# Kernel optimization log

Measured on AMD Instinct MI355X. Metric: run time of the kernel, lower is better.

## Reference

```python
import jax, jax.numpy as jnp
import numpy as np

HIDDEN = 4544
N_HEADS = 71
HEAD_DIM = 64
SEQ = 2048
ROPE_BASE = 10000.0


def _rope_cos_sin(seq_len, dim, base=ROPE_BASE):
    inv_freq = 1.0 / (base ** (jnp.arange(0, dim, 2, dtype=jnp.float32) / dim))
    t = jnp.arange(seq_len, dtype=jnp.float32)
    freqs = jnp.einsum('i,j->ij', t, inv_freq)          # [s, dim/2]
    emb = jnp.concatenate([freqs, freqs], axis=-1)      # [s, dim]
    return jnp.cos(emb), jnp.sin(emb)


def _rotate_half(x):
    x1, x2 = jnp.split(x, 2, axis=-1)
    return jnp.concatenate([-x2, x1], axis=-1)


def _apply_rope(x, cos, sin):
    # x: [..., s, d]; cos/sin: [s, d] broadcast over leading dims
    return x * cos + _rotate_half(x) * sin


def setup_inputs() -> dict:
    key = jax.random.key(0)
    k1, k2, k3 = jax.random.split(key, 3)
    hidden_states = jax.random.normal(k1, (1, 1, SEQ, HIDDEN), dtype=jnp.float32) * 0.02
    qkv_weight = jax.random.normal(k2, ((N_HEADS + 2) * HEAD_DIM, HIDDEN), dtype=jnp.float32) * 0.02
    dense_weight = jax.random.normal(k3, (HIDDEN, HIDDEN), dtype=jnp.float32) * 0.02
    # causal additive mask, same construction as the torch module (triu of -1e5)
    mask = jnp.triu(jnp.full((SEQ, SEQ), -100000.0, dtype=jnp.float32), k=1)[None, None]
    return {
        'hidden_states': hidden_states,
        'qkv_weight': qkv_weight,
        'dense_weight': dense_weight,
        'attention_mask': mask,
    }


def reference(hidden_states, qkv_weight, dense_weight, attention_mask):
    b = hidden_states.shape[0]
    s = hidden_states.shape[2]
    x = hidden_states[:, 0]                                   # [b, s, H]

    # fused QKV projection (no bias): [b, s, (nH+2)*d]
    fused = jnp.einsum('bsh,oh->bso', x, qkv_weight)

    q = fused[..., : N_HEADS * HEAD_DIM]
    q = q.reshape(b, s, N_HEADS, HEAD_DIM).transpose(0, 2, 1, 3)   # [b, nH, s, d]
    k = fused[..., N_HEADS * HEAD_DIM : (N_HEADS + 1) * HEAD_DIM]  # [b, s, d] (single KV head, MQA)
    v = fused[..., (N_HEADS + 1) * HEAD_DIM :]                     # [b, s, d]

    cos, sin = _rope_cos_sin(s, HEAD_DIM)
    q = _apply_rope(q, cos, sin)
    k = _apply_rope(k, cos, sin)

    scale = 1.0 / np.sqrt(HEAD_DIM).astype(np.float32)
    scores = jnp.einsum('bhqd,bkd->bhqk', q, k) * scale            # [b, nH, s, s]
    scores = scores + attention_mask
    attn = jax.nn.softmax(scores, axis=-1)
    out = jnp.einsum('bhqk,bkd->bhqd', attn, v)                    # [b, nH, s, d]

    out = out.transpose(0, 2, 1, 3).reshape(b, s, N_HEADS * HEAD_DIM)  # concat heads
    out = jnp.einsum('bsh,oh->bso', out, dense_weight)             # dense projection
    return out[:, None]                                            # [b, 1, s, H]
```

## Files before the change

### kernel.cpp

```cpp
#include <hip/hip_runtime.h>

#define SEQ     2048
#define HIDDEN  4544
#define NHEAD   71
#define HD      64
#define QKV_OUT 4672

typedef __bf16    bf16;
typedef _Float16  f16;
typedef __bf16    bf16x8 __attribute__((ext_vector_type(8)));
typedef __bf16    bf16x4 __attribute__((ext_vector_type(4)));
typedef _Float16  f16x4  __attribute__((ext_vector_type(4)));
typedef _Float16  f16x8  __attribute__((ext_vector_type(8)));
typedef float     f32x4  __attribute__((ext_vector_type(4)));

__device__ inline void gl2lds16(const void* g, void* ldsbase) {
  __builtin_amdgcn_global_load_lds(
      (const __attribute__((address_space(1))) unsigned int*)g,
      (__attribute__((address_space(3))) unsigned int*)ldsbase,
      16, 0, 0);
}

__global__ void cvt_f32_bf16_k(const float* __restrict__ in, bf16* __restrict__ out, int n4) {
  int i = blockIdx.x * blockDim.x + threadIdx.x;
  if (i >= n4) return;
  float4 f = ((const float4*)in)[i];
  bf16x4 o;
  o[0] = (bf16)f.x; o[1] = (bf16)f.y; o[2] = (bf16)f.z; o[3] = (bf16)f.w;
  *(bf16x4*)(out + (size_t)i * 4) = o;
}

__global__ __launch_bounds__(256) void gemm_bt_k(const bf16* __restrict__ A,
                                                 const bf16* __restrict__ B,
                                                 float* __restrict__ C,
                                                 int K, int Nmat, int ldc) {
  __shared__ bf16 lA[2][128 * 32];
  __shared__ bf16 lB[2][128 * 32];
  const int t = threadIdx.x;
  const int lane = t & 63, w = t >> 6;

  const int gx = gridDim.x;
  const int nwg = gx * gridDim.y;
  const int orig = blockIdx.y * gx + blockIdx.x;
  const int swz = (orig & 7) * (nwg >> 3) + (orig >> 3);
  const int m0 = (swz % gx) * 128;
  const int n0 = (swz / gx) * 128;

  const int wm = (w >> 1) * 64, wn = (w & 1) * 64;
  const int qi = lane & 15, grp = lane >> 4;

  const int r0 = t >> 2;
  const int c0 = (t & 3) * 8;
  const bf16* gA0 = A + (size_t)(m0 + r0) * K + c0;
  const bf16* gA1 = A + (size_t)(m0 + 64 + r0) * K + c0;
  int bR0 = n0 + r0;      if (bR0 >= Nmat) bR0 = Nmat - 1;
  int bR1 = n0 + 64 + r0; if (bR1 >= Nmat) bR1 = Nmat - 1;
  const bf16* gB0 = B + (size_t)bR0 * K + c0;
  const bf16* gB1 = B + (size_t)bR1 * K + c0;
  bf16* lA00 = &lA[0][0] + w * 512;
  bf16* lA01 = &lA[0][2048] + w * 512;
  bf16* lA10 = &lA[1][0] + w * 512;
  bf16* lA11 = &lA[1][2048] + w * 512;
  bf16* lB00 = &lB[0][0] + w * 512;
  bf16* lB01 = &lB[0][2048] + w * 512;
  bf16* lB10 = &lB[1][0] + w * 512;
  bf16* lB11 = &lB[1][2048] + w * 512;

  f32x4 acc[4][4] = {};
  for (int k0 = 0; k0 < K; k0 += 64) {
    __syncthreads();
    gl2lds16(gA0 + k0,      lA00);
    gl2lds16(gA1 + k0,      lA01);
    gl2lds16(gA0 + k0 + 32, lA10);
    gl2lds16(gA1 + k0 + 32, lA11);
    gl2lds16(gB0 + k0,      lB00);
    gl2lds16(gB1 + k0,      lB01);
    gl2lds16(gB0 + k0 + 32, lB10);
    gl2lds16(gB1 + k0 + 32, lB11);
    __syncthreads();
#pragma unroll
    for (int half = 0; half < 2; ++half) {
      bf16x8 af[4], bfv[4];
#pragma unroll
      for (int i = 0; i < 4; ++i)
        af[i] = *(const bf16x8*)&lA[half][(wm + i * 16 + qi) * 32 + grp * 8];
#pragma unroll
      for (int i = 0; i < 4; ++i)
        bfv[i] = *(const bf16x8*)&lB[half][(wn + i * 16 + qi) * 32 + grp * 8];
#pragma unroll
      for (int i = 0; i < 4; ++i)
#pragma unroll
        for (int j = 0; j < 4; ++j)
          acc[i][j] = __builtin_amdgcn_mfma_f32_16x16x32_bf16(af[i], bfv[j], acc[i][j], 0, 0, 0);
    }
  }

#pragma unroll
  for (int i = 0; i < 4; ++i) {
    const int row = m0 + wm + i * 16 + grp * 4;
#pragma unroll
    for (int j = 0; j < 4; ++j) {
      const int col = n0 + wn + j * 16 + qi;
      if (col < Nmat) {
#pragma unroll
        for (int r = 0; r < 4; ++r)
          C[(size_t)(row + r) * ldc + col] = acc[i][j][r];
      }
    }
  }
}

__global__ __launch_bounds__(256) void rope_q_k(const float* __restrict__ fused,
                                                bf16* __restrict__ Qb,
                                                float* __restrict__ cs_tab,
                                                float* __restrict__ sn_tab) {
  const int s = blockIdx.x, t = threadIdx.x;
  __shared__ float cs[64], sn[64];
  if (t < 64) {
    int i = t & 31;
    double invf = pow(10000.0, -(double)i / 32.0);
    double ang = (double)s * invf;
    float c = (float)cos(ang), n = (float)sin(ang);
    cs[t] = c; sn[t] = n;
    cs_tab[s * 64 + t] = c;
    sn_tab[s * 64 + t] = n;
  }
  __syncthreads();
  const float* row = fused + (size_t)s * QKV_OUT;
  for (int e = t; e < HIDDEN; e += 256) {
    int d = e & 63;
    float x = row[e], xp = row[e ^ 32];
    float rot = (d < 32) ? -xp : xp;
    Qb[(size_t)s * HIDDEN + e] = (bf16)((x * cs[d] + rot * sn[d]) * 0.125f);
  }
}

__global__ __launch_bounds__(64) void kvprep_k(const float* __restrict__ fused,
                                               const float* __restrict__ cs_tab,
                                               const float* __restrict__ sn_tab,
                                               bf16* __restrict__ Kf,
                                               f16* __restrict__ Vf) {
  const int t16 = blockIdx.x, lane = threadIdx.x;
  const int qi = lane & 15, grp = lane >> 4;
  const int s = t16 * 16 + qi;
  const float* krow = fused + (size_t)s * QKV_OUT + NHEAD * 64;
  const float* cs = cs_tab + s * 64;
  const float* sn = sn_tab + s * 64;
#pragma unroll
  for (int half = 0; half < 2; ++half) {
    bf16x8 o;
    const int d0 = half * 32 + grp * 8;
#pragma unroll
    for (int j = 0; j < 8; ++j) {
      int d = d0 + j;
      float x = krow[d], xp = krow[d ^ 32];
      float rot = (d < 32) ? -xp : xp;
      o[j] = (bf16)(x * cs[d] + rot * sn[d]);
    }
    *(bf16x8*)&Kf[(t16 * 2 + half) * 512 + lane * 8] = o;
  }
#pragma unroll
  for (int p = 0; p < 2; ++p) {
    f16x8 o;
#pragma unroll
    for (int h = 0; h < 2; ++h) {
      const int tt = p * 2 + h;
#pragma unroll
      for (int j = 0; j < 4; ++j)
        o[h * 4 + j] = (f16)fused[(size_t)(t16 * 16 + grp * 4 + j) * QKV_OUT + (NHEAD + 1) * 64 + tt * 16 + qi];
    }
    *(f16x8*)&Vf[t16 * 1024 + p * 512 + lane * 8] = o;
  }
}

__global__ __launch_bounds__(64) void attn_k(const bf16* __restrict__ Qb,
                                             const bf16* __restrict__ Kf,
                                             const f16*  __restrict__ Vf,
                                             bf16* __restrict__ Ao) {
  __shared__ float fl[2 * 16 * 68];
  const int h = blockIdx.y;
  const int b32 = gridDim.x - 1 - blockIdx.x;
  const int lane = threadIdx.x;
  const int qi = lane & 15, grp = lane >> 4;
  const int q0 = b32 * 32;
  const int lastT = b32 >> 1;

  bf16x8 qf[2][2];
#pragma unroll
  for (int qq = 0; qq < 2; ++qq) {
    const bf16* qb = Qb + (size_t)(q0 + qq * 16 + qi) * HIDDEN + h * 64 + grp * 8;
    qf[qq][0] = *(const bf16x8*)qb;
    qf[qq][1] = *(const bf16x8*)(qb + 32);
  }

  f32x4 o[2][4] = {};
  float l[2] = {0.f, 0.f};

  for (int kb = 0; kb <= lastT; ++kb) {
    const bf16* kfp = Kf + (size_t)kb * 4096 + lane * 8;
    bf16x8 kf[4][2];
#pragma unroll
    for (int kk = 0; kk < 4; ++kk) {
      kf[kk][0] = *(const bf16x8*)(kfp + kk * 1024);
      kf[kk][1] = *(const bf16x8*)(kfp + kk * 1024 + 512);
    }
    f32x4 s4[2][4];
#pragma unroll
    for (int qq = 0; qq < 2; ++qq)
#pragma unroll
      for (int kk = 0; kk < 4; ++kk) {
        f32x4 z = {};
        s4[qq][kk] = __builtin_amdgcn_mfma_f32_16x16x32_bf16(kf[kk][0], qf[qq][0], z, 0, 0, 0);
        s4[qq][kk] = __builtin_amdgcn_mfma_f32_16x16x32_bf16(kf[kk][1], qf[qq][1], s4[qq][kk], 0, 0, 0);
      }
    const f16* vfp = Vf + (size_t)kb * 4096 + lane * 8;
    f16x4 vf[4][4];
#pragma unroll
    for (int kk = 0; kk < 4; ++kk)
#pragma unroll
      for (int p = 0; p < 2; ++p) {
        f16x8 v8 = *(const f16x8*)(vfp + kk * 1024 + p * 512);
#pragma unroll
        for (int j = 0; j < 4; ++j) {
          vf[kk][2 * p][j]     = v8[j];
          vf[kk][2 * p + 1][j] = v8[4 + j];
        }
      }

    if (kb == lastT) {
      const int dq = q0 - kb * 64 + qi;
#pragma unroll
      for (int qq = 0; qq < 2; ++qq)
#pragma unroll
        for (int kk = 0; kk < 4; ++kk)
#pragma unroll
          for (int r = 0; r < 4; ++r)
            if (kk * 16 + grp * 4 + r > dq + qq * 16) s4[qq][kk][r] = -1e30f;
    }
    f16x4 pf[2][4];
#pragma unroll
    for (int qq = 0; qq < 2; ++qq) {
      float ls = 0.f;
#pragma unroll
      for (int kk = 0; kk < 4; ++kk) {
        float p0 = __expf(s4[qq][kk][0]), p1 = __expf(s4[qq][kk][1]);
        float p2 = __expf(s4[qq][kk][2]), p3 = __expf(s4[qq][kk][3]);
        ls += (p0 + p1) + (p2 + p3);
        pf[qq][kk][0] = (f16)p0; pf[qq][kk][1] = (f16)p1;
        pf[qq][kk][2] = (f16)p2; pf[qq][kk][3] = (f16)p3;
      }
      l[qq] += ls;
    }
#pragma unroll
    for (int qq = 0; qq < 2; ++qq)
#pragma unroll
      for (int tt = 0; tt < 4; ++tt)
#pragma unroll
        for (int kk = 0; kk < 4; ++kk)
          o[qq][tt] = __builtin_amdgcn_mfma_f32_16x16x16f16(pf[qq][kk], vf[kk][tt], o[qq][tt], 0, 0, 0);
  }

#pragma unroll
  for (int qq = 0; qq < 2; ++qq) {
    float lq = l[qq];
    lq += __shfl_xor(lq, 16);
    lq += __shfl_xor(lq, 32);
    const float inv = 1.0f / lq;
    const float i0 = __shfl(inv, grp * 4 + 0);
    const float i1 = __shfl(inv, grp * 4 + 1);
    const float i2 = __shfl(inv, grp * 4 + 2);
    const float i3 = __shfl(inv, grp * 4 + 3);
    float* flq = fl + qq * 1088;
#pragma unroll
    for (int tt = 0; tt < 4; ++tt) {
      flq[(grp * 4 + 0) * 68 + tt * 16 + qi] = o[qq][tt][0] * i0;
      flq[(grp * 4 + 1) * 68 + tt * 16 + qi] = o[qq][tt][1] * i1;
      flq[(grp * 4 + 2) * 68 + tt * 16 + qi] = o[qq][tt][2] * i2;
      flq[(grp * 4 + 3) * 68 + tt * 16 + qi] = o[qq][tt][3] * i3;
    }
  }
  __syncthreads();
  const int row = lane >> 2, c0 = (lane & 3) * 16;
#pragma unroll
  for (int qq = 0; qq < 2; ++qq) {
    const float* flq = fl + qq * 1088;
    bf16x8 w0, w1;
#pragma unroll
    for (int j = 0; j < 8; ++j) {
      w0[j] = (bf16)flq[row * 68 + c0 + j];
      w1[j] = (bf16)flq[row * 68 + c0 + 8 + j];
    }
    bf16* ob = Ao + (size_t)(q0 + qq * 16 + row) * HIDDEN + h * 64 + c0;
    *(bf16x8*)ob = w0;
    *(bf16x8*)(ob + 8) = w1;
  }
}

extern "C" void kernel_launch(void* const* d_in, const int* in_sizes, int n_in,
                              void* d_out, int out_size, void* d_ws, size_t ws_size,
                              hipStream_t stream) {
  (void)in_sizes; (void)n_in; (void)out_size; (void)ws_size;
  const float* hs   = (const float*)d_in[0];
  const float* wqkv = (const float*)d_in[1];
  const float* wd   = (const float*)d_in[2];
  float* out = (float*)d_out;

  char* ws = (char*)d_ws;
  size_t off = 0;
  auto alloc = [&](size_t b) -> char* {
    char* p = ws + off;
    off += (b + 255) & ~(size_t)255;
    return p;
  };
  bf16* Xb     = (bf16*)alloc((size_t)SEQ * HIDDEN * 2);
  bf16* Wqb    = (bf16*)alloc((size_t)QKV_OUT * HIDDEN * 2);
  bf16* Wdb    = (bf16*)alloc((size_t)HIDDEN * HIDDEN * 2);
  float* fused = (float*)alloc((size_t)SEQ * QKV_OUT * 4);
  bf16* Qb     = (bf16*)alloc((size_t)SEQ * HIDDEN * 2);
  bf16* Kf     = (bf16*)alloc((size_t)(SEQ / 16) * 1024 * 2);
  f16*  Vf     = (f16*)alloc((size_t)(SEQ / 16) * 1024 * 2);
  float* cs_tab = (float*)alloc((size_t)SEQ * 64 * 4);
  float* sn_tab = (float*)alloc((size_t)SEQ * 64 * 4);
  bf16* Ao     = (bf16*)fused;

  {
    int n4 = SEQ * HIDDEN / 4;
    cvt_f32_bf16_k<<<(n4 + 255) / 256, 256, 0, stream>>>(hs, Xb, n4);
    n4 = QKV_OUT * HIDDEN / 4;
    cvt_f32_bf16_k<<<(n4 + 255) / 256, 256, 0, stream>>>(wqkv, Wqb, n4);
    n4 = HIDDEN * HIDDEN / 4;
    cvt_f32_bf16_k<<<(n4 + 255) / 256, 256, 0, stream>>>(wd, Wdb, n4);
  }
  gemm_bt_k<<<dim3(SEQ / 128, (QKV_OUT + 127) / 128), 256, 0, stream>>>(
      Xb, Wqb, fused, HIDDEN, QKV_OUT, QKV_OUT);
  rope_q_k<<<SEQ, 256, 0, stream>>>(fused, Qb, cs_tab, sn_tab);
  kvprep_k<<<SEQ / 16, 64, 0, stream>>>(fused, cs_tab, sn_tab, Kf, Vf);
  attn_k<<<dim3(SEQ / 32, NHEAD), 64, 0, stream>>>(Qb, Kf, Vf, Ao);
  gemm_bt_k<<<dim3(SEQ / 128, (HIDDEN + 127) / 128), 256, 0, stream>>>(
      Ao, Wdb, out, HIDDEN, HIDDEN, HIDDEN);
}
```

Before: 550.0 us.

## Fuse conversion launches, merge RoPE/KV prep, and use exp2 softmax

The three f32-to-bf16 conversions run in a single launch, and the Q RoPE and K/V layout preparation are fused into one per-row kernel. This removes the cos/sin table round trip and extra launches. The Q RoPE is vectorised with float4 loads that pair each low half with its high half. log2(e) is folded into the Q scale so attention can call exp2f instead of __expf. The fused kernel writes K/V with scattered scalar stores, which may cost some store efficiency.

```diff
diff --git a/kernel.cpp b/kernel.cpp
--- a/kernel.cpp
+++ b/kernel.cpp
@@ -21,13 +21,20 @@
       16, 0, 0);
 }
 
-__global__ void cvt_f32_bf16_k(const float* __restrict__ in, bf16* __restrict__ out, int n4) {
+__global__ void cvt3_k(const float* __restrict__ a, const float* __restrict__ b,
+                       const float* __restrict__ c,
+                       bf16* __restrict__ oa, bf16* __restrict__ ob, bf16* __restrict__ oc,
+                       int na4, int nb4, int nc4) {
   int i = blockIdx.x * blockDim.x + threadIdx.x;
-  if (i >= n4) return;
-  float4 f = ((const float4*)in)[i];
+  const float* src; bf16* dst; int idx;
+  if (i < na4)             { src = a; dst = oa; idx = i; }
+  else if (i < na4 + nb4)  { src = b; dst = ob; idx = i - na4; }
+  else if (i < na4 + nb4 + nc4) { src = c; dst = oc; idx = i - na4 - nb4; }
+  else return;
+  float4 f = ((const float4*)src)[idx];
   bf16x4 o;
   o[0] = (bf16)f.x; o[1] = (bf16)f.y; o[2] = (bf16)f.z; o[3] = (bf16)f.w;
-  *(bf16x4*)(out + (size_t)i * 4) = o;
+  *(bf16x4*)(dst + (size_t)idx * 4) = o;
 }
 
 __global__ __launch_bounds__(256) void gemm_bt_k(const bf16* __restrict__ A,
@@ -110,66 +117,52 @@
   }
 }
 
-__global__ __launch_bounds__(256) void rope_q_k(const float* __restrict__ fused,
+#define QSCALE 0.18033688f
+__global__ __launch_bounds__(256) void ropekv_k(const float* __restrict__ fused,
                                                 bf16* __restrict__ Qb,
-                                                float* __restrict__ cs_tab,
-                                                float* __restrict__ sn_tab) {
+                                                bf16* __restrict__ Kf,
+                                                f16* __restrict__ Vf) {
   const int s = blockIdx.x, t = threadIdx.x;
   __shared__ float cs[64], sn[64];
   if (t < 64) {
     int i = t & 31;
     double invf = pow(10000.0, -(double)i / 32.0);
     double ang = (double)s * invf;
-    float c = (float)cos(ang), n = (float)sin(ang);
-    cs[t] = c; sn[t] = n;
-    cs_tab[s * 64 + t] = c;
-    sn_tab[s * 64 + t] = n;
+    cs[t] = (float)cos(ang);
+    sn[t] = (float)sin(ang);
   }
   __syncthreads();
   const float* row = fused + (size_t)s * QKV_OUT;
-  for (int e = t; e < HIDDEN; e += 256) {
-    int d = e & 63;
-    float x = row[e], xp = row[e ^ 32];
+
+  if (t < 64) {
+    const int d = t;
+    float x = row[NHEAD * 64 + d], xp = row[NHEAD * 64 + (d ^ 32)];
     float rot = (d < 32) ? -xp : xp;
-    Qb[(size_t)s * HIDDEN + e] = (bf16)((x * cs[d] + rot * sn[d]) * 0.125f);
-  }
-}
-
-__global__ __launch_bounds__(64) void kvprep_k(const float* __restrict__ fused,
-                                               const float* __restrict__ cs_tab,
-                                               const float* __restrict__ sn_tab,
-                                               bf16* __restrict__ Kf,
-                                               f16* __restrict__ Vf) {
-  const int t16 = blockIdx.x, lane = threadIdx.x;
-  const int qi = lane & 15, grp = lane >> 4;
-  const int s = t16 * 16 + qi;
-  const float* krow = fused + (size_t)s * QKV_OUT + NHEAD * 64;
-  const float* cs = cs_tab + s * 64;
-  const float* sn = sn_tab + s * 64;
-#pragma unroll
-  for (int half = 0; half < 2; ++half) {
-    bf16x8 o;
-    const int d0 = half * 32 + grp * 8;
-#pragma unroll
-    for (int j = 0; j < 8; ++j) {
-      int d = d0 + j;
-      float x = krow[d], xp = krow[d ^ 32];
-      float rot = (d < 32) ? -xp : xp;
-      o[j] = (bf16)(x * cs[d] + rot * sn[d]);
-    }
-    *(bf16x8*)&Kf[(t16 * 2 + half) * 512 + lane * 8] = o;
-  }
-#pragma unroll
-  for (int p = 0; p < 2; ++p) {
-    f16x8 o;
-#pragma unroll
-    for (int h = 0; h < 2; ++h) {
-      const int tt = p * 2 + h;
-#pragma unroll
-      for (int j = 0; j < 4; ++j)
-        o[h * 4 + j] = (f16)fused[(size_t)(t16 * 16 + grp * 4 + j) * QKV_OUT + (NHEAD + 1) * 64 + tt * 16 + qi];
-    }
-    *(f16x8*)&Vf[t16 * 1024 + p * 512 + lane * 8] = o;
+    Kf[(s >> 4) * 1024 + (d >> 5) * 512 + ((d >> 3) & 3) * 128 + (s & 15) * 8 + (d & 7)] =
+        (bf16)(x * cs[d] + rot * sn[d]);
+  } else if (t < 128) {
+    const int d = t - 64;
+    Vf[(s >> 4) * 1024 + (d >> 5) * 512 + ((s >> 2) & 3) * 128 + (d & 15) * 8 +
+       ((d >> 4) & 1) * 4 + (s & 3)] = (f16)row[(NHEAD + 1) * 64 + d];
+  }
+
+  bf16* qrow = Qb + (size_t)s * HIDDEN;
+  for (int u = t; u < NHEAD * 8; u += 256) {
+    const int head = u >> 3, c4 = (u & 7) * 4;
+    const int e = head * 64 + c4;
+    float4 lo = *(const float4*)(row + e);
+    float4 hi = *(const float4*)(row + e + 32);
+    float xl[4] = {lo.x, lo.y, lo.z, lo.w};
+    float xh[4] = {hi.x, hi.y, hi.z, hi.w};
+    bf16x4 qlo, qhi;
+#pragma unroll
+    for (int j = 0; j < 4; ++j) {
+      const float c = cs[c4 + j], n = sn[c4 + j];
+      qlo[j] = (bf16)((xl[j] * c - xh[j] * n) * QSCALE);
+      qhi[j] = (bf16)((xh[j] * c + xl[j] * n) * QSCALE);
+    }
+    *(bf16x4*)(qrow + e) = qlo;
+    *(bf16x4*)(qrow + e + 32) = qhi;
   }
 }
 
@@ -243,8 +236,8 @@
       float ls = 0.f;
 #pragma unroll
       for (int kk = 0; kk < 4; ++kk) {
-        float p0 = __expf(s4[qq][kk][0]), p1 = __expf(s4[qq][kk][1]);
-        float p2 = __expf(s4[qq][kk][2]), p3 = __expf(s4[qq][kk][3]);
+        float p0 = exp2f(s4[qq][kk][0]), p1 = exp2f(s4[qq][kk][1]);
+        float p2 = exp2f(s4[qq][kk][2]), p3 = exp2f(s4[qq][kk][3]);
         ls += (p0 + p1) + (p2 + p3);
         pf[qq][kk][0] = (f16)p0; pf[qq][kk][1] = (f16)p1;
         pf[qq][kk][2] = (f16)p2; pf[qq][kk][3] = (f16)p3;
@@ -319,22 +312,16 @@
   bf16* Qb     = (bf16*)alloc((size_t)SEQ * HIDDEN * 2);
   bf16* Kf     = (bf16*)alloc((size_t)(SEQ / 16) * 1024 * 2);
   f16*  Vf     = (f16*)alloc((size_t)(SEQ / 16) * 1024 * 2);
-  float* cs_tab = (float*)alloc((size_t)SEQ * 64 * 4);
-  float* sn_tab = (float*)alloc((size_t)SEQ * 64 * 4);
   bf16* Ao     = (bf16*)fused;
 
-  {
-    int n4 = SEQ * HIDDEN / 4;
-    cvt_f32_bf16_k<<<(n4 + 255) / 256, 256, 0, stream>>>(hs, Xb, n4);
-    n4 = QKV_OUT * HIDDEN / 4;
-    cvt_f32_bf16_k<<<(n4 + 255) / 256, 256, 0, stream>>>(wqkv, Wqb, n4);
-    n4 = HIDDEN * HIDDEN / 4;
-    cvt_f32_bf16_k<<<(n4 + 255) / 256, 256, 0, stream>>>(wd, Wdb, n4);
-  }
+  const int na4 = SEQ * HIDDEN / 4;
+  const int nb4 = QKV_OUT * HIDDEN / 4;
+  const int nc4 = HIDDEN * HIDDEN / 4;
+  cvt3_k<<<(na4 + nb4 + nc4 + 255) / 256, 256, 0, stream>>>(
+      hs, wqkv, wd, Xb, Wqb, Wdb, na4, nb4, nc4);
   gemm_bt_k<<<dim3(SEQ / 128, (QKV_OUT + 127) / 128), 256, 0, stream>>>(
       Xb, Wqb, fused, HIDDEN, QKV_OUT, QKV_OUT);
-  rope_q_k<<<SEQ, 256, 0, stream>>>(fused, Qb, cs_tab, sn_tab);
-  kvprep_k<<<SEQ / 16, 64, 0, stream>>>(fused, cs_tab, sn_tab, Kf, Vf);
+  ropekv_k<<<SEQ, 256, 0, stream>>>(fused, Qb, Kf, Vf);
   attn_k<<<dim3(SEQ / 32, NHEAD), 64, 0, stream>>>(Qb, Kf, Vf, Ao);
   gemm_bt_k<<<dim3(SEQ / 128, (HIDDEN + 127) / 128), 256, 0, stream>>>(
       Ao, Wdb, out, HIDDEN, HIDDEN, HIDDEN);
```

Result: slower. 567.5 us (+3.2%).
